# Kernel optimization log

Measured on AMD Instinct MI355X. Metric: run time of the kernel, lower is better.

## Reference

```python
import jax, jax.numpy as jnp
import numpy as np

B, L, D = 2, 2048, 512
NUM_HEADS = 8
LN_EPS = 1e-5


def setup_inputs() -> dict:
    key = jax.random.key(0)
    ks = jax.random.split(key, 4)
    s = 1.0 / np.sqrt(D)
    return {
        "x": jax.random.normal(ks[0], (B, L, D), dtype=jnp.float32),
        "in_proj_w": jax.random.normal(ks[1], (3 * D, D), dtype=jnp.float32) * s,
        "in_proj_b": jnp.zeros((3 * D,), dtype=jnp.float32),
        "out_proj_w": jax.random.normal(ks[2], (D, D), dtype=jnp.float32) * s,
        "out_proj_b": jnp.zeros((D,), dtype=jnp.float32),
        "ln_gamma": jnp.ones((D,), dtype=jnp.float32),
        "ln_beta": jnp.zeros((D,), dtype=jnp.float32),
        "window_size": 10,
    }


def reference(x, in_proj_w, in_proj_b, out_proj_w, out_proj_b, ln_gamma, ln_beta, window_size):
    b, l, d = x.shape
    h = NUM_HEADS
    hd = d // h

    # packed qkv projection (torch Linear: y = x @ W.T + b)
    qkv = x @ in_proj_w.T + in_proj_b  # [B, L, 3D]
    q, k, v = jnp.split(qkv, 3, axis=-1)

    def heads(t):  # [B, L, D] -> [B, H, L, hd]
        return t.reshape(b, l, h, hd).transpose(0, 2, 1, 3)

    q, k, v = heads(q), heads(k), heads(v)
    q = q * (1.0 / np.sqrt(hd))  # torch MHA scales q

    scores = jnp.einsum("bhqd,bhkd->bhqk", q, k)  # [B, H, L, L]

    # Faithful to the source + torch bool attn_mask semantics:
    # mask starts all-True, positions OUTSIDE window set to False;
    # torch masks (=-inf) where the bool mask is True, i.e. INSIDE
    # the window [i - w//2, i + w//2).
    half = window_size // 2
    i = jnp.arange(l)[:, None]
    j = jnp.arange(l)[None, :]
    banned = (j >= i - half) & (j < i + half)  # [L, L] bool
    scores = jnp.where(banned[None, None], -jnp.inf, scores)

    attn = jax.nn.softmax(scores, axis=-1)
    ctx = jnp.einsum("bhqk,bhkd->bhqd", attn, v)  # [B, H, L, hd]
    ctx = ctx.transpose(0, 2, 1, 3).reshape(b, l, d)
    attn_out = ctx @ out_proj_w.T + out_proj_b

    # residual + LayerNorm
    y = x + attn_out
    mu = jnp.mean(y, axis=-1, keepdims=True)
    var = jnp.mean(jnp.square(y - mu), axis=-1, keepdims=True)
    return (y - mu) * jax.lax.rsqrt(var + LN_EPS) * ln_gamma + ln_beta
```

## Files before the change

### kernel.cpp

```cpp
#include <hip/hip_runtime.h>
#include <hip/hip_bf16.h>
#include <math.h>

namespace {

constexpr int Bb = 2, Ll = 2048, Dd = 512, Hh = 8;
constexpr int M = Bb * Ll;
constexpr int THREE_D = 3 * Dd;

typedef __attribute__((ext_vector_type(8))) short short8;
typedef __attribute__((ext_vector_type(4))) short short4v;
typedef __attribute__((ext_vector_type(4))) float f32x4;

__device__ __forceinline__ unsigned short f2bf(float x) {
  union { __hip_bfloat16 h; unsigned short u; } cv;
  cv.h = __float2bfloat16(x);
  return cv.u;
}

__device__ __forceinline__ float fexp2(float x) {
  float r;
  asm("v_exp_f32 %0, %1" : "=v"(r) : "v"(x));
  return r;
}

__device__ __forceinline__ void gload_lds16(const void* g, void* l) {
  __builtin_amdgcn_global_load_lds(
      (const __attribute__((address_space(1))) void*)g,
      (__attribute__((address_space(3))) void*)l, 16, 0, 0);
}

constexpr int QUADS_X = (M * Dd) / 4;
constexpr int QUADS_W1 = (THREE_D * Dd) / 4;
constexpr int QUADS_W2 = (Dd * Dd) / 4;
constexpr int QUADS_TOT = QUADS_X + QUADS_W1 + QUADS_W2;

__global__ __launch_bounds__(256) void cvt_bf16(
    const float* __restrict__ x, const float* __restrict__ w1,
    const float* __restrict__ w2, unsigned short* __restrict__ xb,
    unsigned short* __restrict__ wb, unsigned short* __restrict__ wob) {
  const int i = blockIdx.x * 256 + threadIdx.x;
  const float* src;
  unsigned short* dst;
  if (i < QUADS_X) {
    src = x + 4 * (size_t)i;
    dst = xb + 4 * (size_t)i;
  } else if (i < QUADS_X + QUADS_W1) {
    const int j = i - QUADS_X;
    src = w1 + 4 * (size_t)j;
    dst = wb + 4 * (size_t)j;
  } else {
    const int j = i - (QUADS_X + QUADS_W1);
    src = w2 + 4 * (size_t)j;
    dst = wob + 4 * (size_t)j;
  }
  float4 v = *reinterpret_cast<const float4*>(src);
  ushort4 o;
  o.x = f2bf(v.x); o.y = f2bf(v.y); o.z = f2bf(v.z); o.w = f2bf(v.w);
  *reinterpret_cast<ushort4*>(dst) = o;
}

template <int BM, int K, int N, bool QKV>
__global__ __launch_bounds__(256) void gemm_mfma(
    const unsigned short* __restrict__ A, const unsigned short* __restrict__ B,
    const float* __restrict__ bias, const float* __restrict__ R,
    unsigned short* __restrict__ Cb, float* __restrict__ Cf) {
  __shared__ unsigned short As[BM * 64];
  __shared__ unsigned short Bs[128 * 64];
  constexpr int MF = BM / 32;
  constexpr int AL = BM / 32;

  const int tid = threadIdx.x;
  const int lane = tid & 63;
  const int wu = __builtin_amdgcn_readfirstlane(tid >> 6);
  const int q = lane & 15;
  const int g = lane >> 4;
  const int wr = wu >> 1, wc = wu & 1;
  const int m0 = blockIdx.y * BM, n0 = blockIdx.x * 128;

  const int srow = lane >> 3;
  const int scol = 8 * ((lane & 7) ^ srow);
  const unsigned short* Ag = A + (size_t)(m0 + (BM / 4) * wu + srow) * K + scol;
  const unsigned short* Bg = B + (size_t)(n0 + 32 * wu + srow) * K + scol;
  char* AsW = (char*)As + wu * (BM / 4) * 128;
  char* BsW = (char*)Bs + wu * 4096;

  f32x4 acc[MF][4] = {};

  for (int k0 = 0; k0 < K; k0 += 64) {
    __syncthreads();
#pragma unroll
    for (int i = 0; i < AL; ++i)
      gload_lds16(Ag + (size_t)(8 * i) * K + k0, AsW + 1024 * i);
#pragma unroll
    for (int i = 0; i < 4; ++i)
      gload_lds16(Bg + (size_t)(8 * i) * K + k0, BsW + 1024 * i);
    __syncthreads();

    const char* Abase = (const char*)As + (wr * (BM / 2) + q) * 128;
    const char* Bbase = (const char*)Bs + (wc * 64 + q) * 128;
#pragma unroll
    for (int s = 0; s < 2; ++s) {
      const int csw = (64 * s + 16 * g) ^ ((q & 7) << 4);
      short8 af[MF], bf[4];
#pragma unroll
      for (int m = 0; m < MF; ++m)
        af[m] = *reinterpret_cast<const short8*>(Abase + m * 2048 + csw);
#pragma unroll
      for (int n = 0; n < 4; ++n)
        bf[n] = *reinterpret_cast<const short8*>(Bbase + n * 2048 + csw);
#pragma unroll
      for (int m = 0; m < MF; ++m)
#pragma unroll
        for (int n = 0; n < 4; ++n)
          acc[m][n] = __builtin_amdgcn_mfma_f32_16x16x32_bf16(
              af[m], bf[n], acc[m][n], 0, 0, 0);
    }
  }

  const float sc = (QKV && n0 < Dd) ? 0.125f * 1.44269504f : 1.0f;
#pragma unroll
  for (int m = 0; m < MF; ++m) {
#pragma unroll
    for (int r = 0; r < 4; ++r) {
      const int row = m0 + wr * (BM / 2) + m * 16 + 4 * g + r;
#pragma unroll
      for (int n = 0; n < 4; ++n) {
        const int col = n0 + wc * 64 + n * 16 + q;
        const float v = acc[m][n][r] + bias[col];
        if (QKV) {
          Cb[(size_t)row * N + col] = f2bf(v * sc);
        } else {
          Cf[(size_t)row * N + col] = v + R[(size_t)row * N + col];
        }
      }
    }
  }
}

__global__ __launch_bounds__(512) void attn_mfma(
    const unsigned short* __restrict__ qkv, const int* __restrict__ wsz,
    unsigned short* __restrict__ ctx) {
  __shared__ unsigned short Kls[8192];
  __shared__ unsigned short Vls[8192];
  __shared__ unsigned short Pls[8192];

  const int tid = threadIdx.x;
  const int lane = tid & 63;
  const int w = tid >> 6;
  const int wu = __builtin_amdgcn_readfirstlane(w);
  const int wg = wu & 3;
  const int hv = wu >> 2;
  const int q = lane & 15;
  const int g = lane >> 4;

  const int qt = blockIdx.x & 31;
  const int h = (blockIdx.x >> 5) & 7;
  const int b = blockIdx.x >> 8;
  const int qbase = qt * 64;
  const int hwin = wsz[0] >> 1;

  const size_t bh_base = (size_t)b * Ll * THREE_D + h * 64;

  const unsigned short* qrow =
      qkv + bh_base + (size_t)(qbase + wg * 16 + q) * THREE_D;
  short8 qf0 = *reinterpret_cast<const short8*>(qrow + 8 * g);
  short8 qf1 = *reinterpret_cast<const short8*>(qrow + 32 + 8 * g);
  asm volatile("s_waitcnt vmcnt(0)" : "+v"(qf0), "+v"(qf1)::"memory");

  const int k_rowoff = wg * 16 + (lane >> 3);
  const int k_dcol = 8 * ((lane & 7) ^ ((lane >> 3) & 7));
  const unsigned short* kg_base = qkv + bh_base + Dd + k_dcol;

  const int v_rowoff = 32 * (wg >> 1) + 8 * ((lane >> 4) & 3) +
                       4 * ((lane >> 3) & 1) + ((lane >> 1) & 3);
  const unsigned short* vg_base = qkv + bh_base + 2 * Dd + 8 * (lane & 1);

  unsigned short* kst = &Kls[hv * 4096 + wg * 1024];
  unsigned short* vst = &Vls[hv * 4096 + wg * 1024];
  unsigned short* pw = &Pls[wu * 1024];
  const char* kbytes = (const char*)Kls + hv * 8192;
  const char* vbytes = (const char*)Vls + hv * 8192;
  char* pb = (char*)pw;

  f32x4 oacc[4] = {};
  float m_run = -1e30f, lp = 0.f;

  const int qlo = qbase + wg * 16;
  const int iq = qlo + q;

  for (int t = 0; t < 16; ++t) {
    const int kbase = (hv * 16 + t) * 64;
    __syncthreads();

    gload_lds16(kg_base + (size_t)(kbase + k_rowoff) * THREE_D, kst);
    gload_lds16(kg_base + (size_t)(kbase + k_rowoff + 8) * THREE_D, kst + 512);
    gload_lds16(vg_base + (size_t)(kbase + v_rowoff) * THREE_D +
                    16 * ((2 * wg + 0) & 3), vst);
    gload_lds16(vg_base + (size_t)(kbase + v_rowoff) * THREE_D +
                    16 * ((2 * wg + 1) & 3), vst + 512);
    __syncthreads();

    f32x4 sa[4] = {};
    __builtin_amdgcn_s_setprio(1);
#pragma unroll
    for (int s = 0; s < 2; ++s) {
      const short8 qf = s ? qf1 : qf0;
#pragma unroll
      for (int n = 0; n < 4; ++n) {
        const int baddr =
            (((16 * n + q) * 128 + 64 * s + 16 * g)) ^ ((q & 7) << 4);
        const short8 kf = *reinterpret_cast<const short8*>(kbytes + baddr);
        sa[n] = __builtin_amdgcn_mfma_f32_16x16x32_bf16(kf, qf, sa[n], 0, 0, 0);
      }
    }
    __builtin_amdgcn_s_setprio(0);

    if (kbase + 64 > qlo - hwin && kbase < qlo + 15 + hwin) {
#pragma unroll
      for (int n = 0; n < 4; ++n) {
#pragma unroll
        for (int r = 0; r < 4; ++r) {
          const int j = kbase + 16 * n + 4 * g + r;
          if (j >= iq - hwin && j < iq + hwin) sa[n][r] = -1e30f;
        }
      }
    }

    float mx0 = fmaxf(fmaxf(fmaxf(sa[0][0], sa[0][1]), sa[0][2]), sa[0][3]);
    float mx1 = fmaxf(fmaxf(fmaxf(sa[1][0], sa[1][1]), sa[1][2]), sa[1][3]);
    float mx2 = fmaxf(fmaxf(fmaxf(sa[2][0], sa[2][1]), sa[2][2]), sa[2][3]);
    float mx3 = fmaxf(fmaxf(fmaxf(sa[3][0], sa[3][1]), sa[3][2]), sa[3][3]);
    float mx = fmaxf(fmaxf(fmaxf(mx0, mx1), mx2), mx3);
    mx = fmaxf(mx, __shfl_xor(mx, 16));
    mx = fmaxf(mx, __shfl_xor(mx, 32));

    if (!__all(mx <= m_run + 8.0f)) {
      const float mnew = fmaxf(m_run, mx);
      const float corr = fexp2(m_run - mnew);
      m_run = mnew;
      lp *= corr;
      float corr_o[4];
#pragma unroll
      for (int r = 0; r < 4; ++r) corr_o[r] = __shfl(corr, 4 * g + r, 16);
#pragma unroll
      for (int n = 0; n < 4; ++n)
#pragma unroll
        for (int r = 0; r < 4; ++r) oacc[n][r] *= corr_o[r];
    }

#pragma unroll
    for (int n = 0; n < 4; ++n)
#pragma unroll
      for (int r = 0; r < 4; ++r) sa[n][r] = fexp2(sa[n][r] - m_run);
    const float s0 = (sa[0][0] + sa[0][1]) + (sa[0][2] + sa[0][3]);
    const float s1 = (sa[1][0] + sa[1][1]) + (sa[1][2] + sa[1][3]);
    const float s2 = (sa[2][0] + sa[2][1]) + (sa[2][2] + sa[2][3]);
    const float s3 = (sa[3][0] + sa[3][1]) + (sa[3][2] + sa[3][3]);
    lp += (s0 + s1) + (s2 + s3);

#pragma unroll
    for (int n = 0; n < 4; ++n) {
      uint2 pk;
      pk.x = (unsigned)f2bf(sa[n][0]) | ((unsigned)f2bf(sa[n][1]) << 16);
      pk.y = (unsigned)f2bf(sa[n][2]) | ((unsigned)f2bf(sa[n][3]) << 16);
      *reinterpret_cast<uint2*>(
          pb + q * 128 + ((32 * n + 8 * g) ^ ((q & 7) << 4))) = pk;
    }
    asm volatile("s_waitcnt lgkmcnt(0)" ::: "memory");

#pragma unroll
    for (int s = 0; s < 2; ++s) {
      const short8 pf = *reinterpret_cast<const short8*>(
          pb + q * 128 + ((64 * s + 16 * g) ^ ((q & 7) << 4)));
      short4v vlo[4], vhi[4];
#pragma unroll
      for (int n = 0; n < 4; ++n) {
        const __attribute__((address_space(3))) unsigned short* va =
            (const __attribute__((address_space(3))) unsigned short*)(
                vbytes + 4096 * s + 1024 * n + 256 * g + 8 * q);
        asm volatile("ds_read_b64_tr_b16 %0, %1 offset:0" : "=v"(vlo[n]) : "v"(va));
        asm volatile("ds_read_b64_tr_b16 %0, %1 offset:128" : "=v"(vhi[n]) : "v"(va));
      }
      asm volatile("s_waitcnt lgkmcnt(0)"
                   : "+v"(vlo[0]), "+v"(vhi[0]), "+v"(vlo[1]), "+v"(vhi[1]),
                     "+v"(vlo[2]), "+v"(vhi[2]), "+v"(vlo[3]), "+v"(vhi[3])
                   :
                   : "memory");
      __builtin_amdgcn_sched_barrier(0);
      __builtin_amdgcn_s_setprio(1);
#pragma unroll
      for (int n = 0; n < 4; ++n) {
        const short8 vf =
            __builtin_shufflevector(vlo[n], vhi[n], 0, 1, 2, 3, 4, 5, 6, 7);
        oacc[n] = __builtin_amdgcn_mfma_f32_16x16x32_bf16(pf, vf, oacc[n], 0, 0, 0);
      }
      __builtin_amdgcn_s_setprio(0);
    }
  }

  lp += __shfl_xor(lp, 16);
  lp += __shfl_xor(lp, 32);
  const float l_run = lp;

  float* Om = (float*)Kls;
  float* mls = (float*)Vls;

  __syncthreads();
  if (w >= 4) {
#pragma unroll
    for (int r = 0; r < 4; ++r) {
      const int rr = wg * 16 + 4 * g + r;
#pragma unroll
      for (int n = 0; n < 4; ++n) Om[rr * 64 + 16 * n + q] = oacc[n][r];
    }
    if (g == 0)
      *reinterpret_cast<float2*>(&mls[(wg * 16 + q) * 2]) =
          make_float2(m_run, l_run);
  }
  __syncthreads();
  if (w < 4) {
#pragma unroll
    for (int r = 0; r < 4; ++r) {
      const int rr = wg * 16 + 4 * g + r;
      const float m_own = __shfl(m_run, 4 * g + r, 16);
      const float l_own = __shfl(l_run, 4 * g + r, 16);
      const float2 ml2 = *reinterpret_cast<const float2*>(&mls[rr * 2]);
      const float ms = fmaxf(m_own, ml2.x);
      const float c1 = fexp2(m_own - ms);
      const float c2 = fexp2(ml2.x - ms);
      const float inv = 1.0f / (c1 * l_own + c2 * ml2.y);
      const int row = qbase + rr;
      unsigned short* crow = ctx + ((size_t)(b * Ll + row)) * Dd + h * 64 + q;
#pragma unroll
      for (int n = 0; n < 4; ++n) {
        const float o2 = Om[rr * 64 + 16 * n + q];
        crow[16 * n] = f2bf((c1 * oacc[n][r] + c2 * o2) * inv);
      }
    }
  }
}

__global__ __launch_bounds__(256) void ln_kernel(
    const float* __restrict__ y, const float* __restrict__ gamma,
    const float* __restrict__ beta, float* __restrict__ out) {
  const int row = blockIdx.x;
  const int tid = threadIdx.x;
  const float* yr = y + (size_t)row * Dd;

  float2 v = *reinterpret_cast<const float2*>(&yr[tid * 2]);
  float s = v.x + v.y;
  float qq = v.x * v.x + v.y * v.y;
#pragma unroll
  for (int off = 1; off < 64; off <<= 1) {
    s += __shfl_xor(s, off, 64);
    qq += __shfl_xor(qq, off, 64);
  }
  __shared__ float ss[4], qs[4];
  if ((tid & 63) == 0) { ss[tid >> 6] = s; qs[tid >> 6] = qq; }
  __syncthreads();
  s = (ss[0] + ss[1]) + (ss[2] + ss[3]);
  qq = (qs[0] + qs[1]) + (qs[2] + qs[3]);

  const float mu = s * (1.0f / Dd);
  const float var = qq * (1.0f / Dd) - mu * mu;
  const float rstd = rsqrtf(var + 1e-5f);

  float2 gmv = *reinterpret_cast<const float2*>(&gamma[tid * 2]);
  float2 bev = *reinterpret_cast<const float2*>(&beta[tid * 2]);
  float2 o;
  o.x = (v.x - mu) * rstd * gmv.x + bev.x;
  o.y = (v.y - mu) * rstd * gmv.y + bev.y;
  *reinterpret_cast<float2*>(&out[(size_t)row * Dd + tid * 2]) = o;
}

}

extern "C" void kernel_launch(void* const* d_in, const int* in_sizes, int n_in,
                              void* d_out, int out_size, void* d_ws,
                              size_t ws_size, hipStream_t stream) {
  const float* x = (const float*)d_in[0];
  const float* w_in = (const float*)d_in[1];
  const float* b_in = (const float*)d_in[2];
  const float* w_out = (const float*)d_in[3];
  const float* b_out = (const float*)d_in[4];
  const float* gamma = (const float*)d_in[5];
  const float* beta = (const float*)d_in[6];
  const int* wsz = (const int*)d_in[7];
  float* out = (float*)d_out;

  unsigned short* ws16 = (unsigned short*)d_ws;
  unsigned short* qkvb = ws16;
  unsigned short* ctxb = ws16 + 6291456;
  unsigned short* xb = ws16 + 8388608;
  unsigned short* wb = ws16 + 10485760;
  unsigned short* wob = ws16 + 11272192;
  float* y = (float*)d_ws;

  dim3 blk(256);

  cvt_bf16<<<dim3(QUADS_TOT / 256), blk, 0, stream>>>(x, w_in, w_out, xb, wb,
                                                      wob);
  gemm_mfma<64, 512, 1536, true><<<dim3(12, 64), blk, 0, stream>>>(
      xb, wb, b_in, nullptr, qkvb, nullptr);
  attn_mfma<<<dim3(512), dim3(512), 0, stream>>>(qkvb, wsz, ctxb);
  gemm_mfma<64, 512, 512, false><<<dim3(4, 64), blk, 0, stream>>>(
      ctxb, wob, b_out, x, nullptr, y);
  ln_kernel<<<dim3(M), blk, 0, stream>>>(y, gamma, beta, out);
}
```

Before: 73.52 us.

## Process 128-key blocks per iteration in windowed attention kernel

Doubles the key/value tile each loop iteration from 64 to 128 keys, which halves the iterations and the __syncthreads pairs. It also halves the online-softmax max/rescale steps. K and V shared memory are doubled to hold both sub-tiles. The cost is more LDS use (64KB plus P) and more registers for the 8 score accumulators, which may lower occupancy.

```diff
diff --git a/kernel.cpp b/kernel.cpp
--- a/kernel.cpp
+++ b/kernel.cpp
@@ -141,8 +141,8 @@
 __global__ __launch_bounds__(512) void attn_mfma(
     const unsigned short* __restrict__ qkv, const int* __restrict__ wsz,
     unsigned short* __restrict__ ctx) {
-  __shared__ unsigned short Kls[8192];
-  __shared__ unsigned short Vls[8192];
+  __shared__ unsigned short Kls[16384];
+  __shared__ unsigned short Vls[16384];
   __shared__ unsigned short Pls[8192];
 
   const int tid = threadIdx.x;
@@ -176,11 +176,11 @@
                        4 * ((lane >> 3) & 1) + ((lane >> 1) & 3);
   const unsigned short* vg_base = qkv + bh_base + 2 * Dd + 8 * (lane & 1);
 
-  unsigned short* kst = &Kls[hv * 4096 + wg * 1024];
-  unsigned short* vst = &Vls[hv * 4096 + wg * 1024];
+  unsigned short* kst = &Kls[hv * 8192 + wg * 1024];
+  unsigned short* vst = &Vls[hv * 8192 + wg * 1024];
   unsigned short* pw = &Pls[wu * 1024];
-  const char* kbytes = (const char*)Kls + hv * 8192;
-  const char* vbytes = (const char*)Vls + hv * 8192;
+  const char* kbytes = (const char*)Kls + hv * 16384;
+  const char* vbytes = (const char*)Vls + hv * 16384;
   char* pb = (char*)pw;
 
   f32x4 oacc[4] = {};
@@ -189,36 +189,43 @@
   const int qlo = qbase + wg * 16;
   const int iq = qlo + q;
 
-  for (int t = 0; t < 16; ++t) {
-    const int kbase = (hv * 16 + t) * 64;
+  for (int t = 0; t < 8; ++t) {
+    const int kbase = hv * 1024 + t * 128;
     __syncthreads();
 
-    gload_lds16(kg_base + (size_t)(kbase + k_rowoff) * THREE_D, kst);
-    gload_lds16(kg_base + (size_t)(kbase + k_rowoff + 8) * THREE_D, kst + 512);
-    gload_lds16(vg_base + (size_t)(kbase + v_rowoff) * THREE_D +
-                    16 * ((2 * wg + 0) & 3), vst);
-    gload_lds16(vg_base + (size_t)(kbase + v_rowoff) * THREE_D +
-                    16 * ((2 * wg + 1) & 3), vst + 512);
+#pragma unroll
+    for (int u = 0; u < 2; ++u) {
+      const int kb = kbase + u * 64;
+      gload_lds16(kg_base + (size_t)(kb + k_rowoff) * THREE_D, kst + u * 4096);
+      gload_lds16(kg_base + (size_t)(kb + k_rowoff + 8) * THREE_D,
+                  kst + u * 4096 + 512);
+      gload_lds16(vg_base + (size_t)(kb + v_rowoff) * THREE_D +
+                      16 * ((2 * wg + 0) & 3), vst + u * 4096);
+      gload_lds16(vg_base + (size_t)(kb + v_rowoff) * THREE_D +
+                      16 * ((2 * wg + 1) & 3), vst + u * 4096 + 512);
+    }
     __syncthreads();
 
-    f32x4 sa[4] = {};
+    f32x4 sa[8] = {};
     __builtin_amdgcn_s_setprio(1);
 #pragma unroll
     for (int s = 0; s < 2; ++s) {
       const short8 qf = s ? qf1 : qf0;
 #pragma unroll
-      for (int n = 0; n < 4; ++n) {
+      for (int n = 0; n < 8; ++n) {
+        const int u = n >> 2, nn = n & 3;
         const int baddr =
-            (((16 * n + q) * 128 + 64 * s + 16 * g)) ^ ((q & 7) << 4);
+            u * 8192 + ((((16 * nn + q) * 128 + 64 * s + 16 * g)) ^
+                        ((q & 7) << 4));
         const short8 kf = *reinterpret_cast<const short8*>(kbytes + baddr);
         sa[n] = __builtin_amdgcn_mfma_f32_16x16x32_bf16(kf, qf, sa[n], 0, 0, 0);
       }
     }
     __builtin_amdgcn_s_setprio(0);
 
-    if (kbase + 64 > qlo - hwin && kbase < qlo + 15 + hwin) {
-#pragma unroll
-      for (int n = 0; n < 4; ++n) {
+    if (kbase + 128 > qlo - hwin && kbase < qlo + 15 + hwin) {
+#pragma unroll
+      for (int n = 0; n < 8; ++n) {
 #pragma unroll
         for (int r = 0; r < 4; ++r) {
           const int j = kbase + 16 * n + 4 * g + r;
@@ -227,11 +234,13 @@
       }
     }
 
-    float mx0 = fmaxf(fmaxf(fmaxf(sa[0][0], sa[0][1]), sa[0][2]), sa[0][3]);
-    float mx1 = fmaxf(fmaxf(fmaxf(sa[1][0], sa[1][1]), sa[1][2]), sa[1][3]);
-    float mx2 = fmaxf(fmaxf(fmaxf(sa[2][0], sa[2][1]), sa[2][2]), sa[2][3]);
-    float mx3 = fmaxf(fmaxf(fmaxf(sa[3][0], sa[3][1]), sa[3][2]), sa[3][3]);
-    float mx = fmaxf(fmaxf(fmaxf(mx0, mx1), mx2), mx3);
+    float mxa[8];
+#pragma unroll
+    for (int n = 0; n < 8; ++n)
+      mxa[n] = fmaxf(fmaxf(fmaxf(sa[n][0], sa[n][1]), sa[n][2]), sa[n][3]);
+    float mx = fmaxf(
+        fmaxf(fmaxf(mxa[0], mxa[1]), fmaxf(mxa[2], mxa[3])),
+        fmaxf(fmaxf(mxa[4], mxa[5]), fmaxf(mxa[6], mxa[7])));
     mx = fmaxf(mx, __shfl_xor(mx, 16));
     mx = fmaxf(mx, __shfl_xor(mx, 32));
 
@@ -250,52 +259,55 @@
     }
 
 #pragma unroll
-    for (int n = 0; n < 4; ++n)
+    for (int n = 0; n < 8; ++n)
 #pragma unroll
       for (int r = 0; r < 4; ++r) sa[n][r] = fexp2(sa[n][r] - m_run);
-    const float s0 = (sa[0][0] + sa[0][1]) + (sa[0][2] + sa[0][3]);
-    const float s1 = (sa[1][0] + sa[1][1]) + (sa[1][2] + sa[1][3]);
-    const float s2 = (sa[2][0] + sa[2][1]) + (sa[2][2] + sa[2][3]);
-    const float s3 = (sa[3][0] + sa[3][1]) + (sa[3][2] + sa[3][3]);
-    lp += (s0 + s1) + (s2 + s3);
-
-#pragma unroll
-    for (int n = 0; n < 4; ++n) {
-      uint2 pk;
-      pk.x = (unsigned)f2bf(sa[n][0]) | ((unsigned)f2bf(sa[n][1]) << 16);
-      pk.y = (unsigned)f2bf(sa[n][2]) | ((unsigned)f2bf(sa[n][3]) << 16);
-      *reinterpret_cast<uint2*>(
-          pb + q * 128 + ((32 * n + 8 * g) ^ ((q & 7) << 4))) = pk;
-    }
-    asm volatile("s_waitcnt lgkmcnt(0)" ::: "memory");
-
-#pragma unroll
-    for (int s = 0; s < 2; ++s) {
-      const short8 pf = *reinterpret_cast<const short8*>(
-          pb + q * 128 + ((64 * s + 16 * g) ^ ((q & 7) << 4)));
-      short4v vlo[4], vhi[4];
+#pragma unroll
+    for (int n = 0; n < 8; ++n)
+      lp += (sa[n][0] + sa[n][1]) + (sa[n][2] + sa[n][3]);
+
+#pragma unroll
+    for (int u = 0; u < 2; ++u) {
 #pragma unroll
       for (int n = 0; n < 4; ++n) {
-        const __attribute__((address_space(3))) unsigned short* va =
-            (const __attribute__((address_space(3))) unsigned short*)(
-                vbytes + 4096 * s + 1024 * n + 256 * g + 8 * q);
-        asm volatile("ds_read_b64_tr_b16 %0, %1 offset:0" : "=v"(vlo[n]) : "v"(va));
-        asm volatile("ds_read_b64_tr_b16 %0, %1 offset:128" : "=v"(vhi[n]) : "v"(va));
-      }
-      asm volatile("s_waitcnt lgkmcnt(0)"
-                   : "+v"(vlo[0]), "+v"(vhi[0]), "+v"(vlo[1]), "+v"(vhi[1]),
-                     "+v"(vlo[2]), "+v"(vhi[2]), "+v"(vlo[3]), "+v"(vhi[3])
-                   :
-                   : "memory");
-      __builtin_amdgcn_sched_barrier(0);
-      __builtin_amdgcn_s_setprio(1);
-#pragma unroll
-      for (int n = 0; n < 4; ++n) {
-        const short8 vf =
-            __builtin_shufflevector(vlo[n], vhi[n], 0, 1, 2, 3, 4, 5, 6, 7);
-        oacc[n] = __builtin_amdgcn_mfma_f32_16x16x32_bf16(pf, vf, oacc[n], 0, 0, 0);
-      }
-      __builtin_amdgcn_s_setprio(0);
+        const f32x4 sv = sa[4 * u + n];
+        uint2 pk;
+        pk.x = (unsigned)f2bf(sv[0]) | ((unsigned)f2bf(sv[1]) << 16);
+        pk.y = (unsigned)f2bf(sv[2]) | ((unsigned)f2bf(sv[3]) << 16);
+        *reinterpret_cast<uint2*>(
+            pb + q * 128 + ((32 * n + 8 * g) ^ ((q & 7) << 4))) = pk;
+      }
+      asm volatile("s_waitcnt lgkmcnt(0)" ::: "memory");
+
+#pragma unroll
+      for (int s = 0; s < 2; ++s) {
+        const short8 pf = *reinterpret_cast<const short8*>(
+            pb + q * 128 + ((64 * s + 16 * g) ^ ((q & 7) << 4)));
+        short4v vlo[4], vhi[4];
+#pragma unroll
+        for (int n = 0; n < 4; ++n) {
+          const __attribute__((address_space(3))) unsigned short* va =
+              (const __attribute__((address_space(3))) unsigned short*)(
+                  vbytes + u * 8192 + 4096 * s + 1024 * n + 256 * g + 8 * q);
+          asm volatile("ds_read_b64_tr_b16 %0, %1 offset:0" : "=v"(vlo[n]) : "v"(va));
+          asm volatile("ds_read_b64_tr_b16 %0, %1 offset:128" : "=v"(vhi[n]) : "v"(va));
+        }
+        asm volatile("s_waitcnt lgkmcnt(0)"
+                     : "+v"(vlo[0]), "+v"(vhi[0]), "+v"(vlo[1]), "+v"(vhi[1]),
+                       "+v"(vlo[2]), "+v"(vhi[2]), "+v"(vlo[3]), "+v"(vhi[3])
+                     :
+                     : "memory");
+        __builtin_amdgcn_sched_barrier(0);
+        __builtin_amdgcn_s_setprio(1);
+#pragma unroll
+        for (int n = 0; n < 4; ++n) {
+          const short8 vf = __builtin_shufflevector(vlo[n], vhi[n], 0, 1, 2, 3,
+                                                    4, 5, 6, 7);
+          oacc[n] =
+              __builtin_amdgcn_mfma_f32_16x16x32_bf16(pf, vf, oacc[n], 0, 0, 0);
+        }
+        __builtin_amdgcn_s_setprio(0);
+      }
     }
   }
 
```

After: 72.68 us (median of 2 runs). About the same (-1.1%).

## Double-buffer K/V LDS tiles in attention kernel to overlap loads with compute

Applied to the files above, without the earlier changes.

Doubles the K and V shared-memory buffers and prefetches the next key/value tile with direct global-to-LDS loads while the current tile is processed, waiting with a partial vmcnt. The goal is to hide global load latency behind the QK and PV MFMA work instead of serializing load then compute each iteration. It doubles K/V LDS usage, which may lower occupancy. It also depends on raw s_barrier and vmcnt accounting being correct for buffer reuse.

```diff
diff --git a/kernel.cpp b/kernel.cpp
--- a/kernel.cpp
+++ b/kernel.cpp
@@ -141,8 +141,8 @@
 __global__ __launch_bounds__(512) void attn_mfma(
     const unsigned short* __restrict__ qkv, const int* __restrict__ wsz,
     unsigned short* __restrict__ ctx) {
-  __shared__ unsigned short Kls[8192];
-  __shared__ unsigned short Vls[8192];
+  __shared__ unsigned short Kls[16384];
+  __shared__ unsigned short Vls[16384];
   __shared__ unsigned short Pls[8192];
 
   const int tid = threadIdx.x;
@@ -176,11 +176,7 @@
                        4 * ((lane >> 3) & 1) + ((lane >> 1) & 3);
   const unsigned short* vg_base = qkv + bh_base + 2 * Dd + 8 * (lane & 1);
 
-  unsigned short* kst = &Kls[hv * 4096 + wg * 1024];
-  unsigned short* vst = &Vls[hv * 4096 + wg * 1024];
   unsigned short* pw = &Pls[wu * 1024];
-  const char* kbytes = (const char*)Kls + hv * 8192;
-  const char* vbytes = (const char*)Vls + hv * 8192;
   char* pb = (char*)pw;
 
   f32x4 oacc[4] = {};
@@ -189,17 +185,39 @@
   const int qlo = qbase + wg * 16;
   const int iq = qlo + q;
 
+#define STAGE(tile, buf)                                                     \
+  {                                                                          \
+    const int kb_ = hv * 1024 + (tile) * 64;                                 \
+    unsigned short* kd_ = &Kls[(buf) * 8192 + hv * 4096 + wg * 1024];        \
+    unsigned short* vd_ = &Vls[(buf) * 8192 + hv * 4096 + wg * 1024];        \
+    gload_lds16(kg_base + (size_t)(kb_ + k_rowoff) * THREE_D, kd_);          \
+    gload_lds16(kg_base + (size_t)(kb_ + k_rowoff + 8) * THREE_D,            \
+                kd_ + 512);                                                  \
+    gload_lds16(vg_base + (size_t)(kb_ + v_rowoff) * THREE_D +               \
+                    16 * ((2 * wg + 0) & 3), vd_);                           \
+    gload_lds16(vg_base + (size_t)(kb_ + v_rowoff) * THREE_D +               \
+                    16 * ((2 * wg + 1) & 3), vd_ + 512);                     \
+  }
+
+  STAGE(0, 0);
+
   for (int t = 0; t < 16; ++t) {
+    const int cur = t & 1;
     const int kbase = (hv * 16 + t) * 64;
-    __syncthreads();
-
-    gload_lds16(kg_base + (size_t)(kbase + k_rowoff) * THREE_D, kst);
-    gload_lds16(kg_base + (size_t)(kbase + k_rowoff + 8) * THREE_D, kst + 512);
-    gload_lds16(vg_base + (size_t)(kbase + v_rowoff) * THREE_D +
-                    16 * ((2 * wg + 0) & 3), vst);
-    gload_lds16(vg_base + (size_t)(kbase + v_rowoff) * THREE_D +
-                    16 * ((2 * wg + 1) & 3), vst + 512);
-    __syncthreads();
+
+    __builtin_amdgcn_s_barrier();
+
+    if (t < 15) {
+      STAGE(t + 1, cur ^ 1);
+      asm volatile("s_waitcnt vmcnt(4)" ::: "memory");
+    } else {
+      asm volatile("s_waitcnt vmcnt(0)" ::: "memory");
+    }
+    __builtin_amdgcn_s_barrier();
+    asm volatile("" ::: "memory");
+
+    const char* kbytes = (const char*)Kls + cur * 16384 + hv * 8192;
+    const char* vbytes = (const char*)Vls + cur * 16384 + hv * 8192;
 
     f32x4 sa[4] = {};
     __builtin_amdgcn_s_setprio(1);
@@ -298,6 +316,7 @@
       __builtin_amdgcn_s_setprio(0);
     }
   }
+#undef STAGE
 
   lp += __shfl_xor(lp, 16);
   lp += __shfl_xor(lp, 32);
```

Result: slower. 75.46 us (+2.6%).
